# Kernel tuning notes

Hardware: AMD Instinct MI355X
Metric: run time of the kernel (lower is better)

## Reference

```python
import jax, jax.numpy as jnp
import numpy as np
from jax.ops import segment_sum

I_N, K_T, J_F, D, L, E, NT, H = 100000, 128, 64, 128, 2, 1000000, 500000, 2


def setup_inputs() -> dict:
    key = jax.random.key(0)
    ks = jax.random.split(key, 32)
    def rn(k, shp, s=0.02):
        return jax.random.normal(k, shp, jnp.float32) * s
    inp = {}
    inp["edge_x"] = jax.random.normal(ks[0], (E, J_F), jnp.float32)
    inp["edge_i"] = jax.random.randint(ks[1], (E,), 0, I_N, jnp.int32)
    inp["edge_k"] = jax.random.randint(ks[2], (E,), 0, K_T, jnp.int32)
    inp["idx_i"] = jax.random.randint(ks[3], (NT,), 0, I_N, jnp.int32)
    inp["idx_j"] = jax.random.randint(ks[4], (NT,), 0, J_F, jnp.int32)
    inp["idx_k"] = jax.random.randint(ks[5], (NT,), 0, K_T, jnp.int32)
    # parameters
    inp["u0"] = rn(ks[6], (I_N, D))          # Embedding(I,dim), xavier-ish
    inp["w0"] = rn(ks[7], (K_T, D), 0.01)
    inp["ep_W"] = rn(ks[8], (J_F, D))        # edge_proj (stored [in,out])
    inp["ep_b"] = jnp.zeros((D,), jnp.float32)
    inp["uW"] = rn(ks[9], (L, 2 * D, D))
    inp["ub"] = jnp.zeros((L, D), jnp.float32)
    inp["wW"] = rn(ks[10], (L, 2 * D, D))
    inp["wb"] = jnp.zeros((L, D), jnp.float32)
    inp["pos"] = rn(ks[11], (K_T, D), 0.01)
    inp["Wq"] = rn(ks[12], (D, D)); inp["Wk"] = rn(ks[13], (D, D)); inp["Wv"] = rn(ks[14], (D, D))
    inp["bq"] = jnp.zeros((D,), jnp.float32); inp["bk"] = jnp.zeros((D,), jnp.float32); inp["bv"] = jnp.zeros((D,), jnp.float32)
    inp["Wo"] = rn(ks[15], (D, D)); inp["bo"] = jnp.zeros((D,), jnp.float32)
    inp["ln1_g"] = jnp.ones((D,), jnp.float32); inp["ln1_b"] = jnp.zeros((D,), jnp.float32)
    inp["f_W1"] = rn(ks[16], (D, 4 * D)); inp["f_b1"] = jnp.zeros((4 * D,), jnp.float32)
    inp["f_W2"] = rn(ks[17], (4 * D, D)); inp["f_b2"] = jnp.zeros((D,), jnp.float32)
    inp["ln2_g"] = jnp.ones((D,), jnp.float32); inp["ln2_b"] = jnp.zeros((D,), jnp.float32)
    inp["V"] = rn(ks[18], (J_F, D))
    inp["bias"] = jnp.zeros((1,), jnp.float32)
    return inp


def _ln(x, g, b, eps=1e-5):
    m = jnp.mean(x, -1, keepdims=True)
    v = jnp.mean((x - m) ** 2, -1, keepdims=True)
    return (x - m) * jax.lax.rsqrt(v + eps) * g + b


def reference(edge_x, edge_i, edge_k, idx_i, idx_j, idx_k, u0, w0, ep_W, ep_b,
              uW, ub, wW, wb, pos, Wq, Wk, Wv, bq, bk, bv, Wo, bo,
              ln1_g, ln1_b, f_W1, f_b1, f_W2, f_b2, ln2_g, ln2_b, V, bias):
    I, K = u0.shape[0], w0.shape[0]
    e = edge_x @ ep_W + ep_b                                   # [E,D] edge_proj (same every layer)
    ones = jnp.ones((edge_i.shape[0],), jnp.float32)
    cnt_u = jnp.clip(segment_sum(ones, edge_i, num_segments=I), 1.0)[:, None]
    cnt_w = jnp.clip(segment_sum(ones, edge_k, num_segments=K), 1.0)[:, None]
    U, W = u0, w0
    for l in range(uW.shape[0]):
        U_msg = segment_sum(W[edge_k] + e, edge_i, num_segments=I)
        W_msg = segment_sum(U[edge_i] + e, edge_k, num_segments=K)
        U = jax.nn.relu(jnp.concatenate([U, U_msg / cnt_u], 1) @ uW[l] + ub[l])
        W = jax.nn.relu(jnp.concatenate([W, W_msg / cnt_w], 1) @ wW[l] + wb[l])
    # TimeRefine: MHA over K time tokens
    dh = D // H
    X = W + pos                                                # [K,D]
    q = (X @ Wq + bq).reshape(K, H, dh)
    k_ = (X @ Wk + bk).reshape(K, H, dh)
    v = (X @ Wv + bv).reshape(K, H, dh)
    scores = jnp.einsum('qhd,khd->hqk', q, k_) / jnp.sqrt(jnp.float32(dh))
    attn = jnp.einsum('hqk,khd->qhd', jax.nn.softmax(scores, -1), v).reshape(K, D)
    attn = attn @ Wo + bo
    H1 = _ln(X + attn, ln1_g, ln1_b)
    H2 = jax.nn.relu(H1 @ f_W1 + f_b1) @ f_W2 + f_b2
    Wf = _ln(H1 + H2, ln2_g, ln2_b)
    # decode triples
    s = U[idx_i] * Wf[idx_k]                                   # [N,D]
    out = jnp.sum(s * V[idx_j], -1) + bias[0]
    return jax.nn.sigmoid(out)
```

## Files before the change

kernel.cpp:

```cpp
#include <hip/hip_runtime.h>
#include <hip/hip_bf16.h>

#define D_DIM 128
#define KT 128
#define JF 64
#define WB_BLOCKS 256

typedef __attribute__((ext_vector_type(8))) short bf16x8;
typedef __attribute__((ext_vector_type(4))) float f32x4;

__device__ inline unsigned short f2b(float f) {
    __hip_bfloat16 h = __float2bfloat16(f);
    return *reinterpret_cast<unsigned short*>(&h);
}
__device__ inline float b2f(unsigned short u) {
    unsigned int x = ((unsigned int)u) << 16;
    return __uint_as_float(x);
}

__global__ void __launch_bounds__(256) edge_pass_kernel(
    const float* __restrict__ edge_x, const int* __restrict__ edge_i,
    const int* __restrict__ edge_k, float* __restrict__ Xi, float* __restrict__ Xk,
    unsigned* __restrict__ NmatP, unsigned* __restrict__ cntw, int E, int epb)
{
    __shared__ float xk_s[KT * JF];
    __shared__ unsigned cw_s[KT];
    for (int t = threadIdx.x; t < KT * JF; t += 256) xk_s[t] = 0.f;
    if (threadIdx.x < KT) cw_s[threadIdx.x] = 0u;
    __syncthreads();
    const int wid = threadIdx.x >> 6, lane = threadIdx.x & 63;
    const long base = (long)blockIdx.x * epb;
    for (int c = wid; c < epb; c += 4) {
        long e = base + c;
        if (e >= (long)E) break;
        int i = edge_i[e], k = edge_k[e];
        float x = edge_x[e * 64 + lane];
        unsafeAtomicAdd(&Xi[(long)i * 64 + lane], x);
        unsafeAtomicAdd(&xk_s[k * 64 + lane], x);
        if (lane == 0) atomicAdd(&NmatP[(long)i * 32 + (k >> 2)], 1u << ((k & 3) * 8));
        if (lane == 1) atomicAdd(&cw_s[k], 1u);
    }
    __syncthreads();
    for (int t = threadIdx.x; t < KT * JF; t += 256) {
        float v = xk_s[t];
        if (v != 0.f) unsafeAtomicAdd(&Xk[t], v);
    }
    if (threadIdx.x < KT && cw_s[threadIdx.x]) atomicAdd(&cntw[threadIdx.x], cw_s[threadIdx.x]);
}

__global__ void __launch_bounds__(256) mid_kernel(
    const unsigned* __restrict__ NmatP, float* __restrict__ cntraw,
    float* __restrict__ invcnt, int nNodes, int cntB,
    const float* __restrict__ u0, unsigned short* __restrict__ U0b, long n4,
    const float* __restrict__ uWt, const float* __restrict__ Wl,
    const float* __restrict__ uWb, const float* __restrict__ ep_W,
    const float* __restrict__ ep_b,
    unsigned short* __restrict__ Bt, float* __restrict__ ebx)
{
    const int bid = blockIdx.x;
    if (bid < cntB) {
        int row = bid * 4 + (threadIdx.x >> 6);
        int lane = threadIdx.x & 63;
        if (row < nNodes && lane < 32) {
            unsigned wv = NmatP[(long)row * 32 + lane];
            unsigned s = (wv & 0xFF) + ((wv >> 8) & 0xFF) + ((wv >> 16) & 0xFF) + (wv >> 24);
            #pragma unroll
            for (int o = 16; o; o >>= 1) s += __shfl_down(s, o, 32);
            if (lane == 0) {
                float c = (float)s;
                cntraw[row] = c;
                invcnt[row] = 1.f / fmaxf(c, 1.f);
            }
        }
    } else if (bid < cntB + 1024) {
        long i = (long)(bid - cntB) * 256 + threadIdx.x;
        long stride = (long)1024 * 256;
        for (; i < n4; i += stride) {
            float4 v = *(const float4*)&u0[i * 4];
            ushort4 o = make_ushort4(f2b(v.x), f2b(v.y), f2b(v.z), f2b(v.w));
            *(ushort4*)&U0b[i * 4] = o;
        }
    } else {
        int idx = (bid - cntB - 1024) * 256 + threadIdx.x;
        if (idx < 128 * 320) {
            int n = idx / 320, kk = idx - n * 320;
            float v;
            if (kk < 128) {
                v = uWt[kk * 128 + n];
            } else {
                const float* a = (kk < 256) ? (Wl + (kk - 128) * 128) : (ep_W + (kk - 256) * 128);
                float s = 0.f;
                #pragma unroll 8
                for (int j = 0; j < 128; ++j) s += a[j] * uWb[j * 128 + n];
                v = s;
            }
            Bt[idx] = f2b(v);
        } else if (idx < 128 * 320 + 128) {
            int n = idx - 128 * 320;
            float s = 0.f;
            #pragma unroll 8
            for (int j = 0; j < 128; ++j) s += ep_b[j] * uWb[j * 128 + n];
            ebx[n] = s;
        }
    }
}

__global__ void prep_kernel(const float* __restrict__ uWt, const float* __restrict__ Wl,
                            const float* __restrict__ uWb, const float* __restrict__ ep_W,
                            const float* __restrict__ ep_b,
                            unsigned short* __restrict__ Bt, float* __restrict__ ebx)
{
    int idx = blockIdx.x * 256 + threadIdx.x;
    if (idx < 128 * 320) {
        int n = idx / 320, kk = idx - n * 320;
        float v;
        if (kk < 128) {
            v = uWt[kk * 128 + n];
        } else {
            const float* a = (kk < 256) ? (Wl + (kk - 128) * 128) : (ep_W + (kk - 256) * 128);
            float s = 0.f;
            #pragma unroll 8
            for (int j = 0; j < 128; ++j) s += a[j] * uWb[j * 128 + n];
            v = s;
        }
        Bt[idx] = f2b(v);
    } else if (idx < 128 * 320 + 128) {
        int n = idx - 128 * 320;
        float s = 0.f;
        #pragma unroll 8
        for (int j = 0; j < 128; ++j) s += ep_b[j] * uWb[j * 128 + n];
        ebx[n] = s;
    }
}

__global__ void __launch_bounds__(256) layerA_mfma(
    const unsigned short* __restrict__ U_in, const unsigned char* __restrict__ Nmat8,
    const float* __restrict__ Xi, const float* __restrict__ cntraw,
    const float* __restrict__ invcnt, const unsigned short* __restrict__ Bt,
    const float* __restrict__ ub_l, const float* __restrict__ ebx,
    unsigned short* __restrict__ U_out, int nNodes)
{
    __shared__ __align__(16) unsigned short A_s[128][40];
    __shared__ __align__(16) unsigned short B_s[128][40];
    const int tid = threadIdx.x;
    const int w = tid >> 6, lane = tid & 63;
    const int quad = lane >> 4, l16 = lane & 15;
    const int nodeBase = blockIdx.x * 128;
    f32x4 acc[2][8];
    #pragma unroll
    for (int a = 0; a < 2; ++a)
        #pragma unroll
        for (int b = 0; b < 8; ++b) acc[a][b] = (f32x4){0.f, 0.f, 0.f, 0.f};

    const int rr = tid >> 3;
    const int kc = (tid & 7) * 4;

    for (int ks = 0; ks < 10; ++ks) {
        const int k0 = ks * 32;
        __syncthreads();
        {
            int n = tid & 127, seg = tid >> 7;
            const unsigned short* src = Bt + n * 320 + k0 + seg * 16;
            uint4 p0 = *(const uint4*)(src);
            uint4 p1 = *(const uint4*)(src + 8);
            *(uint4*)&B_s[n][seg * 16]     = p0;
            *(uint4*)&B_s[n][seg * 16 + 8] = p1;
        }
        #pragma unroll
        for (int p = 0; p < 4; ++p) {
            int r = p * 32 + rr;
            int node = nodeBase + r;
            ushort4 w4 = make_ushort4(0, 0, 0, 0);
            if (node < nNodes) {
                if (ks < 4) {
                    w4 = *(const ushort4*)&U_in[(long)node * 128 + k0 + kc];
                } else if (ks < 8) {
                    float inv = invcnt[node];
                    const unsigned char* np_ = &Nmat8[(long)node * 128 + (k0 - 128) + kc];
                    w4 = make_ushort4(f2b((float)np_[0] * inv), f2b((float)np_[1] * inv),
                                      f2b((float)np_[2] * inv), f2b((float)np_[3] * inv));
                } else {
                    float inv = invcnt[node];
                    float4 x = *(const float4*)&Xi[(long)node * 64 + (k0 - 256) + kc];
                    w4 = make_ushort4(f2b(x.x * inv), f2b(x.y * inv),
                                      f2b(x.z * inv), f2b(x.w * inv));
                }
            }
            *(ushort4*)&A_s[r][kc] = w4;
        }
        __syncthreads();
        bf16x8 a0 = *(const bf16x8*)&A_s[w * 32 + l16][quad * 8];
        bf16x8 a1 = *(const bf16x8*)&A_s[w * 32 + 16 + l16][quad * 8];
        #pragma unroll
        for (int nt = 0; nt < 8; ++nt) {
            bf16x8 b = *(const bf16x8*)&B_s[nt * 16 + l16][quad * 8];
            acc[0][nt] = __builtin_amdgcn_mfma_f32_16x16x32_bf16(a0, b, acc[0][nt], 0, 0, 0);
            acc[1][nt] = __builtin_amdgcn_mfma_f32_16x16x32_bf16(a1, b, acc[1][nt], 0, 0, 0);
        }
    }
    #pragma unroll
    for (int mt = 0; mt < 2; ++mt) {
        #pragma unroll
        for (int r = 0; r < 4; ++r) {
            int row = w * 32 + mt * 16 + quad * 4 + r;
            int node = nodeBase + row;
            if (node < nNodes) {
                float flag = (cntraw[node] > 0.f) ? 1.f : 0.f;
                #pragma unroll
                for (int nt = 0; nt < 8; ++nt) {
                    int col = nt * 16 + l16;
                    float vv = acc[mt][nt][r] + ub_l[col] + flag * ebx[col];
                    U_out[(long)node * 128 + col] = f2b(fmaxf(vv, 0.f));
                }
            }
        }
    }
}

__global__ void __launch_bounds__(256) wmsgB_mfma(
    const unsigned short* __restrict__ U, const unsigned char* __restrict__ Nmat8,
    float* __restrict__ partial, int nodes_per_block, int nNodes)
{
    __shared__ __align__(16) unsigned short A_s[128][40];
    __shared__ __align__(16) unsigned short B_s[128][40];
    const int tid = threadIdx.x;
    const int w = tid >> 6, lane = tid & 63;
    const int quad = lane >> 4, l16 = lane & 15;
    f32x4 acc[2][8];
    #pragma unroll
    for (int a = 0; a < 2; ++a)
        #pragma unroll
        for (int b = 0; b < 8; ++b) acc[a][b] = (f32x4){0.f, 0.f, 0.f, 0.f};

    int base = blockIdx.x * nodes_per_block;
    int end = min(base + nodes_per_block, nNodes);
    const int nn = tid >> 3;
    const int cc = (tid & 7) * 16;
    for (int g = base; g < end; g += 32) {
        int cnt = min(32, end - g);
        __syncthreads();
        if (nn < cnt) {
            int node = g + nn;
            uint4 nb = *(const uint4*)&Nmat8[(long)node * 128 + cc];
            const unsigned char* nbp = (const unsigned char*)&nb;
            uint4 ua = *(const uint4*)&U[(long)node * 128 + cc];
            uint4 ubb = *(const uint4*)&U[(long)node * 128 + cc + 8];
            unsigned short uv[16];
            *(uint4*)&uv[0] = ua;
            *(uint4*)&uv[8] = ubb;
            #pragma unroll
            for (int j = 0; j < 16; ++j) {
                A_s[cc + j][nn] = f2b((float)nbp[j]);
                B_s[cc + j][nn] = uv[j];
            }
        } else {
            #pragma unroll
            for (int j = 0; j < 16; ++j) { A_s[cc + j][nn] = 0; B_s[cc + j][nn] = 0; }
        }
        __syncthreads();
        bf16x8 a0 = *(const bf16x8*)&A_s[w * 32 + l16][quad * 8];
        bf16x8 a1 = *(const bf16x8*)&A_s[w * 32 + 16 + l16][quad * 8];
        #pragma unroll
        for (int nt = 0; nt < 8; ++nt) {
            bf16x8 b = *(const bf16x8*)&B_s[nt * 16 + l16][quad * 8];
            acc[0][nt] = __builtin_amdgcn_mfma_f32_16x16x32_bf16(a0, b, acc[0][nt], 0, 0, 0);
            acc[1][nt] = __builtin_amdgcn_mfma_f32_16x16x32_bf16(a1, b, acc[1][nt], 0, 0, 0);
        }
    }
    float* my = partial + (size_t)blockIdx.x * 16384;
    #pragma unroll
    for (int mt = 0; mt < 2; ++mt)
        #pragma unroll
        for (int r = 0; r < 4; ++r) {
            int row = w * 32 + mt * 16 + quad * 4 + r;
            #pragma unroll
            for (int nt = 0; nt < 8; ++nt)
                my[row * 128 + nt * 16 + l16] = acc[mt][nt][r];
        }
}

__global__ void __launch_bounds__(128) wfin_gemm_kernel(
    const float* __restrict__ partial, const float* __restrict__ Xk,
    const unsigned* __restrict__ cntw, const float* __restrict__ ep_W,
    const float* __restrict__ ep_b, const float* __restrict__ Wrow,
    const float* __restrict__ wWt, const float* __restrict__ wWb,
    const float* __restrict__ wb_l, float* __restrict__ Wout)
{
    __shared__ float msg_s[128];
    __shared__ float a_s[128];
    const int kk = blockIdx.x, t = threadIdx.x;
    float c = (float)cntw[kk];
    {
        float s = 0.f;
        const float* pp = partial + kk * 128 + t;
        #pragma unroll 8
        for (int b = 0; b < WB_BLOCKS; ++b) s += pp[(size_t)b * 16384];
        const float* xk = Xk + kk * 64;
        #pragma unroll 8
        for (int j = 0; j < 64; ++j) s += xk[j] * ep_W[j * 128 + t];
        s += c * ep_b[t];
        msg_s[t] = s / fmaxf(c, 1.f);
        a_s[t] = Wrow[kk * 128 + t];
    }
    __syncthreads();
    float s = wb_l[t];
    #pragma unroll 4
    for (int k = 0; k < 128; ++k) s += a_s[k] * wWt[k * 128 + t];
    #pragma unroll 4
    for (int k = 0; k < 128; ++k) s += msg_s[k] * wWb[k * 128 + t];
    Wout[kk * 128 + t] = fmaxf(s, 0.f);
}

__global__ void qkvf_kernel(const float* __restrict__ W2, const float* __restrict__ pos,
                            const float* __restrict__ Wq, const float* __restrict__ Wk,
                            const float* __restrict__ Wv, const float* __restrict__ bq,
                            const float* __restrict__ bk, const float* __restrict__ bv,
                            float* __restrict__ Xmat,
                            float* __restrict__ qm, float* __restrict__ km, float* __restrict__ vm)
{
    int idx = blockIdx.x * 256 + threadIdx.x;
    if (idx >= 128 * 384) return;
    int m = idx / 384, c = idx - m * 384;
    int sel = c >> 7, n = c & 127;
    const float* W = (sel == 0) ? Wq : (sel == 1) ? Wk : Wv;
    const float* b = (sel == 0) ? bq : (sel == 1) ? bk : bv;
    float s = b[n];
    const float* x2 = W2 + m * 128;
    const float* xp = pos + m * 128;
    #pragma unroll 8
    for (int k = 0; k < 128; ++k) s += (x2[k] + xp[k]) * W[k * 128 + n];
    float* o = (sel == 0) ? qm : (sel == 1) ? km : vm;
    o[m * 128 + n] = s;
    if (sel == 0) Xmat[m * 128 + n] = x2[n] + xp[n];
}

__global__ void __launch_bounds__(128) attn_tail_kernel(
    const float* __restrict__ q, const float* __restrict__ kmat,
    const float* __restrict__ vmat, const float* __restrict__ Wo,
    const float* __restrict__ bo, const float* __restrict__ Xmat,
    const float* __restrict__ ln1_g, const float* __restrict__ ln1_b,
    const float* __restrict__ f_W1, const float* __restrict__ f_b1,
    const float* __restrict__ f_W2, const float* __restrict__ f_b2,
    const float* __restrict__ ln2_g, const float* __restrict__ ln2_b,
    float* __restrict__ Wf)
{
    __shared__ float p_s[128];
    __shared__ float a_s[128];
    __shared__ float h1_s[128];
    __shared__ float f_s[512];
    __shared__ float red_s[4];
    const int tok = blockIdx.x;
    const int t = threadIdx.x;
    const int lane = t & 63, wid = t >> 6;
    for (int h = 0; h < 2; ++h) {
        const float* qr = q + tok * 128 + h * 64;
        const float* kr = kmat + t * 128 + h * 64;
        float s = 0.f;
        #pragma unroll
        for (int d = 0; d < 64; ++d) s += qr[d] * kr[d];
        s *= 0.125f;
        float m = s;
        #pragma unroll
        for (int o = 32; o; o >>= 1) m = fmaxf(m, __shfl_down(m, o, 64));
        if (lane == 0) red_s[wid] = m;
        __syncthreads();
        m = fmaxf(red_s[0], red_s[1]);
        float ev = expf(s - m);
        float ss = ev;
        #pragma unroll
        for (int o = 32; o; o >>= 1) ss += __shfl_down(ss, o, 64);
        if (lane == 0) red_s[2 + wid] = ss;
        __syncthreads();
        float tot = red_s[2] + red_s[3];
        p_s[t] = ev / tot;
        __syncthreads();
        if (t < 64) {
            float o = 0.f;
            #pragma unroll 8
            for (int j = 0; j < 128; ++j) o += p_s[j] * vmat[j * 128 + h * 64 + t];
            a_s[h * 64 + t] = o;
        }
        __syncthreads();
    }
    {
        float v = bo[t];
        #pragma unroll 4
        for (int k = 0; k < 128; ++k) v += a_s[k] * Wo[k * 128 + t];
        v += Xmat[tok * 128 + t];
        float s = v;
        #pragma unroll
        for (int o = 32; o; o >>= 1) s += __shfl_down(s, o, 64);
        if (lane == 0) red_s[wid] = s;
        __syncthreads();
        float mean = (red_s[0] + red_s[1]) * (1.f / 128.f);
        float d = v - mean;
        float q2 = d * d;
        #pragma unroll
        for (int o = 32; o; o >>= 1) q2 += __shfl_down(q2, o, 64);
        if (lane == 0) red_s[2 + wid] = q2;
        __syncthreads();
        float var = (red_s[2] + red_s[3]) * (1.f / 128.f);
        h1_s[t] = d * rsqrtf(var + 1e-5f) * ln1_g[t] + ln1_b[t];
        __syncthreads();
    }
    #pragma unroll
    for (int nn = 0; nn < 4; ++nn) {
        int n = t + nn * 128;
        float s = f_b1[n];
        #pragma unroll 4
        for (int k = 0; k < 128; ++k) s += h1_s[k] * f_W1[k * 512 + n];
        f_s[n] = fmaxf(s, 0.f);
    }
    __syncthreads();
    float v = f_b2[t];
    #pragma unroll 4
    for (int k = 0; k < 512; ++k) v += f_s[k] * f_W2[k * 128 + t];
    v += h1_s[t];
    float s = v;
    #pragma unroll
    for (int o = 32; o; o >>= 1) s += __shfl_down(s, o, 64);
    if (lane == 0) red_s[wid] = s;
    __syncthreads();
    float mean = (red_s[0] + red_s[1]) * (1.f / 128.f);
    float d = v - mean;
    float q2 = d * d;
    #pragma unroll
    for (int o = 32; o; o >>= 1) q2 += __shfl_down(q2, o, 64);
    if (lane == 0) red_s[2 + wid] = q2;
    __syncthreads();
    float var = (red_s[2] + red_s[3]) * (1.f / 128.f);
    Wf[tok * 128 + t] = d * rsqrtf(var + 1e-5f) * ln2_g[t] + ln2_b[t];
}

__global__ void __launch_bounds__(256) decode_kernel(
    const int* __restrict__ idx_i, const int* __restrict__ idx_j, const int* __restrict__ idx_k,
    const unsigned short* __restrict__ U2, const float* __restrict__ Wf, const float* __restrict__ V,
    const float* __restrict__ bias, float* __restrict__ out, int n)
{
    const int g = threadIdx.x >> 4;
    const int hl = threadIdx.x & 15;
    int t = blockIdx.x * 16 + g;
    if (t >= n) return;
    int i = idx_i[t], j = idx_j[t], kk = idx_k[t];
    const unsigned short* up = U2 + (long)i * 128 + hl * 8;
    const float* wp = Wf + kk * 128 + hl * 8;
    const float* vp = V + j * 128 + hl * 8;
    uint4 ur = *(const uint4*)up;
    const unsigned short* uu = (const unsigned short*)&ur;
    float4 w0 = *(const float4*)wp,  w1 = *(const float4*)(wp + 4);
    float4 v0 = *(const float4*)vp,  v1 = *(const float4*)(vp + 4);
    float s = b2f(uu[0]) * w0.x * v0.x + b2f(uu[1]) * w0.y * v0.y
            + b2f(uu[2]) * w0.z * v0.z + b2f(uu[3]) * w0.w * v0.w
            + b2f(uu[4]) * w1.x * v1.x + b2f(uu[5]) * w1.y * v1.y
            + b2f(uu[6]) * w1.z * v1.z + b2f(uu[7]) * w1.w * v1.w;
    #pragma unroll
    for (int o = 8; o; o >>= 1) s += __shfl_down(s, o, 16);
    if (hl == 0) out[t] = 1.f / (1.f + expf(-(s + bias[0])));
}

extern "C" void kernel_launch(void* const* d_in, const int* in_sizes, int n_in,
                              void* d_out, int out_size, void* d_ws, size_t ws_size,
                              hipStream_t stream)
{
    const float* edge_x = (const float*)d_in[0];
    const int*   edge_i = (const int*)d_in[1];
    const int*   edge_k = (const int*)d_in[2];
    const int*   idx_i  = (const int*)d_in[3];
    const int*   idx_j  = (const int*)d_in[4];
    const int*   idx_k  = (const int*)d_in[5];
    const float* u0   = (const float*)d_in[6];
    const float* w0   = (const float*)d_in[7];
    const float* ep_W = (const float*)d_in[8];
    const float* ep_b = (const float*)d_in[9];
    const float* uW   = (const float*)d_in[10];
    const float* ub   = (const float*)d_in[11];
    const float* wW   = (const float*)d_in[12];
    const float* wb   = (const float*)d_in[13];
    const float* pos  = (const float*)d_in[14];
    const float* Wq = (const float*)d_in[15];
    const float* Wk = (const float*)d_in[16];
    const float* Wv = (const float*)d_in[17];
    const float* bq = (const float*)d_in[18];
    const float* bk = (const float*)d_in[19];
    const float* bv = (const float*)d_in[20];
    const float* Wo = (const float*)d_in[21];
    const float* bo = (const float*)d_in[22];
    const float* ln1_g = (const float*)d_in[23];
    const float* ln1_b = (const float*)d_in[24];
    const float* f_W1 = (const float*)d_in[25];
    const float* f_b1 = (const float*)d_in[26];
    const float* f_W2 = (const float*)d_in[27];
    const float* f_b2 = (const float*)d_in[28];
    const float* ln2_g = (const float*)d_in[29];
    const float* ln2_b = (const float*)d_in[30];
    const float* Vmat = (const float*)d_in[31];
    const float* bias = (const float*)d_in[32];

    const int E   = in_sizes[1];
    const int NTt = in_sizes[3];
    const int nNodes = in_sizes[6] / D_DIM;

    char* ws = (char*)d_ws;
    size_t off = 0;
    auto alloc = [&](size_t bytes) -> char* {
        char* p = ws + off;
        off = (off + bytes + 255) & ~(size_t)255;
        return p;
    };
    unsigned* NmatP  = (unsigned*)alloc((size_t)nNodes * 32 * 4);
    float*    Xi     = (float*)alloc((size_t)nNodes * 64 * 4);
    float*    Xkseg  = (float*)alloc(128 * 64 * 4);
    unsigned* cntw   = (unsigned*)alloc(512);
    size_t zeroBytes = off;
    float* cntraw = (float*)alloc((size_t)nNodes * 4);
    float* invcnt = (float*)alloc((size_t)nNodes * 4);
    unsigned short* U0b = (unsigned short*)alloc((size_t)nNodes * 128 * 2);
    unsigned short* U1b = (unsigned short*)alloc((size_t)nNodes * 128 * 2);
    unsigned short* U2b = (unsigned short*)alloc((size_t)nNodes * 128 * 2);
    float* partials = (float*)alloc((size_t)WB_BLOCKS * 16384 * 4);
    unsigned short* Bt0 = (unsigned short*)alloc(128 * 320 * 2);
    unsigned short* Bt1 = (unsigned short*)alloc(128 * 320 * 2);
    float* W1 = (float*)alloc(65536);
    float* W2 = (float*)alloc(65536);
    float* ebx0 = (float*)alloc(512);
    float* ebx1 = (float*)alloc(512);
    float* Xmat  = (float*)alloc(65536);
    float* qm    = (float*)alloc(65536);
    float* km    = (float*)alloc(65536);
    float* vm    = (float*)alloc(65536);
    float* Wfm   = (float*)alloc(65536);

    const unsigned char* Nmat8 = (const unsigned char*)NmatP;

    const float* uWt0 = uW;
    const float* uWb0 = uW + 128 * 128;
    const float* uWt1 = uW + 256 * 128;
    const float* uWb1 = uW + 256 * 128 + 128 * 128;
    const float* wWt0 = wW;
    const float* wWb0 = wW + 128 * 128;
    const float* wWt1 = wW + 256 * 128;
    const float* wWb1 = wW + 256 * 128 + 128 * 128;

    hipMemsetAsync(d_ws, 0, zeroBytes, stream);

    int epb = (E + 1023) / 1024;
    edge_pass_kernel<<<1024, 256, 0, stream>>>(edge_x, edge_i, edge_k, Xi, Xkseg,
                                               NmatP, cntw, E, epb);

    int cntB = (nNodes + 3) / 4;
    mid_kernel<<<cntB + 1024 + 161, 256, 0, stream>>>(
        NmatP, cntraw, invcnt, nNodes, cntB,
        u0, U0b, (long)nNodes * 32,
        uWt0, w0, uWb0, ep_W, ep_b, Bt0, ebx0);

    int npb = (nNodes + WB_BLOCKS - 1) / WB_BLOCKS;
    int la_grid = (nNodes + 127) / 128;

    wmsgB_mfma<<<WB_BLOCKS, 256, 0, stream>>>(U0b, Nmat8, partials, npb, nNodes);
    layerA_mfma<<<la_grid, 256, 0, stream>>>(U0b, Nmat8, Xi, cntraw, invcnt, Bt0, ub, ebx0, U1b, nNodes);
    wfin_gemm_kernel<<<128, 128, 0, stream>>>(partials, Xkseg, cntw, ep_W, ep_b,
                                              w0, wWt0, wWb0, wb, W1);

    prep_kernel<<<161, 256, 0, stream>>>(uWt1, W1, uWb1, ep_W, ep_b, Bt1, ebx1);
    wmsgB_mfma<<<WB_BLOCKS, 256, 0, stream>>>(U1b, Nmat8, partials, npb, nNodes);
    layerA_mfma<<<la_grid, 256, 0, stream>>>(U1b, Nmat8, Xi, cntraw, invcnt, Bt1, ub + 128, ebx1, U2b, nNodes);
    wfin_gemm_kernel<<<128, 128, 0, stream>>>(partials, Xkseg, cntw, ep_W, ep_b,
                                              W1, wWt1, wWb1, wb + 128, W2);

    qkvf_kernel<<<192, 256, 0, stream>>>(W2, pos, Wq, Wk, Wv, bq, bk, bv, Xmat, qm, km, vm);
    attn_tail_kernel<<<128, 128, 0, stream>>>(qm, km, vm, Wo, bo, Xmat, ln1_g, ln1_b,
                                              f_W1, f_b1, f_W2, f_b2, ln2_g, ln2_b, Wfm);

    decode_kernel<<<(NTt + 15) / 16, 256, 0, stream>>>(idx_i, idx_j, idx_k, U2b, Wfm, Vmat,
                                                       bias, (float*)d_out, NTt);
}
```

Measured before the change: 1.139 ms.

## Fuse edge pass with prep, merge wmsg/layerA kernels, bf16 packed atomics for Xi

The edge scatter is merged with the u0 bf16 conversion and the weight-prep work for both layers into one launch. The counting step is split into its own small kernel. The W-message and U-layer MFMA kernels are combined into a single dual-role grid. Xi is now accumulated with packed bf16 atomics, which halves atomic traffic and footprint but lowers accumulation precision. Layer-1 Bt prep now happens inside wfin_gemm, which removes the separate prep launch and lets independent work overlap instead of running serially.

```diff
diff --git a/kernel.cpp b/kernel.cpp
--- a/kernel.cpp
+++ b/kernel.cpp
@@ -18,112 +18,35 @@
     return __uint_as_float(x);
 }
 
-__global__ void __launch_bounds__(256) edge_pass_kernel(
-    const float* __restrict__ edge_x, const int* __restrict__ edge_i,
-    const int* __restrict__ edge_k, float* __restrict__ Xi, float* __restrict__ Xk,
-    unsigned* __restrict__ NmatP, unsigned* __restrict__ cntw, int E, int epb)
-{
-    __shared__ float xk_s[KT * JF];
-    __shared__ unsigned cw_s[KT];
-    for (int t = threadIdx.x; t < KT * JF; t += 256) xk_s[t] = 0.f;
-    if (threadIdx.x < KT) cw_s[threadIdx.x] = 0u;
-    __syncthreads();
-    const int wid = threadIdx.x >> 6, lane = threadIdx.x & 63;
-    const long base = (long)blockIdx.x * epb;
-    for (int c = wid; c < epb; c += 4) {
-        long e = base + c;
-        if (e >= (long)E) break;
-        int i = edge_i[e], k = edge_k[e];
-        float x = edge_x[e * 64 + lane];
-        unsafeAtomicAdd(&Xi[(long)i * 64 + lane], x);
-        unsafeAtomicAdd(&xk_s[k * 64 + lane], x);
-        if (lane == 0) atomicAdd(&NmatP[(long)i * 32 + (k >> 2)], 1u << ((k & 3) * 8));
-        if (lane == 1) atomicAdd(&cw_s[k], 1u);
-    }
-    __syncthreads();
-    for (int t = threadIdx.x; t < KT * JF; t += 256) {
-        float v = xk_s[t];
-        if (v != 0.f) unsafeAtomicAdd(&Xk[t], v);
-    }
-    if (threadIdx.x < KT && cw_s[threadIdx.x]) atomicAdd(&cntw[threadIdx.x], cw_s[threadIdx.x]);
-}
-
-__global__ void __launch_bounds__(256) mid_kernel(
-    const unsigned* __restrict__ NmatP, float* __restrict__ cntraw,
-    float* __restrict__ invcnt, int nNodes, int cntB,
-    const float* __restrict__ u0, unsigned short* __restrict__ U0b, long n4,
-    const float* __restrict__ uWt, const float* __restrict__ Wl,
-    const float* __restrict__ uWb, const float* __restrict__ ep_W,
-    const float* __restrict__ ep_b,
-    unsigned short* __restrict__ Bt, float* __restrict__ ebx)
-{
-    const int bid = blockIdx.x;
-    if (bid < cntB) {
-        int row = bid * 4 + (threadIdx.x >> 6);
-        int lane = threadIdx.x & 63;
-        if (row < nNodes && lane < 32) {
-            unsigned wv = NmatP[(long)row * 32 + lane];
-            unsigned s = (wv & 0xFF) + ((wv >> 8) & 0xFF) + ((wv >> 16) & 0xFF) + (wv >> 24);
-            #pragma unroll
-            for (int o = 16; o; o >>= 1) s += __shfl_down(s, o, 32);
-            if (lane == 0) {
-                float c = (float)s;
-                cntraw[row] = c;
-                invcnt[row] = 1.f / fmaxf(c, 1.f);
-            }
-        }
-    } else if (bid < cntB + 1024) {
-        long i = (long)(bid - cntB) * 256 + threadIdx.x;
-        long stride = (long)1024 * 256;
-        for (; i < n4; i += stride) {
-            float4 v = *(const float4*)&u0[i * 4];
-            ushort4 o = make_ushort4(f2b(v.x), f2b(v.y), f2b(v.z), f2b(v.w));
-            *(ushort4*)&U0b[i * 4] = o;
-        }
-    } else {
-        int idx = (bid - cntB - 1024) * 256 + threadIdx.x;
-        if (idx < 128 * 320) {
-            int n = idx / 320, kk = idx - n * 320;
-            float v;
-            if (kk < 128) {
-                v = uWt[kk * 128 + n];
-            } else {
-                const float* a = (kk < 256) ? (Wl + (kk - 128) * 128) : (ep_W + (kk - 256) * 128);
+__device__ inline void atomPkAddBf16(unsigned short* addr, unsigned packed) {
+    asm volatile("global_atomic_pk_add_bf16 %0, %1, off"
+                 :: "v"(addr), "v"(packed) : "memory");
+}
+
+__device__ inline void prep_body(int idx, const float* uWt, const float* Wl,
+                                 const float* uWb, const float* ep_W,
+                                 const float* ep_b, unsigned short* Bt,
+                                 float* ebx)
+{
+    if (idx < 128 * 320) {
+        int n = idx / 320, kk = idx - n * 320;
+        if (kk < 128) {
+            Bt[idx] = f2b(uWt[kk * 128 + n]);
+        } else if (kk < 256) {
+            if (Wl) {
+                const float* a = Wl + (kk - 128) * 128;
                 float s = 0.f;
                 #pragma unroll 8
                 for (int j = 0; j < 128; ++j) s += a[j] * uWb[j * 128 + n];
-                v = s;
-            }
-            Bt[idx] = f2b(v);
-        } else if (idx < 128 * 320 + 128) {
-            int n = idx - 128 * 320;
-            float s = 0.f;
-            #pragma unroll 8
-            for (int j = 0; j < 128; ++j) s += ep_b[j] * uWb[j * 128 + n];
-            ebx[n] = s;
-        }
-    }
-}
-
-__global__ void prep_kernel(const float* __restrict__ uWt, const float* __restrict__ Wl,
-                            const float* __restrict__ uWb, const float* __restrict__ ep_W,
-                            const float* __restrict__ ep_b,
-                            unsigned short* __restrict__ Bt, float* __restrict__ ebx)
-{
-    int idx = blockIdx.x * 256 + threadIdx.x;
-    if (idx < 128 * 320) {
-        int n = idx / 320, kk = idx - n * 320;
-        float v;
-        if (kk < 128) {
-            v = uWt[kk * 128 + n];
+                Bt[idx] = f2b(s);
+            }
         } else {
-            const float* a = (kk < 256) ? (Wl + (kk - 128) * 128) : (ep_W + (kk - 256) * 128);
+            const float* a = ep_W + (kk - 256) * 128;
             float s = 0.f;
             #pragma unroll 8
             for (int j = 0; j < 128; ++j) s += a[j] * uWb[j * 128 + n];
-            v = s;
-        }
-        Bt[idx] = f2b(v);
+            Bt[idx] = f2b(s);
+        }
     } else if (idx < 128 * 320 + 128) {
         int n = idx - 128 * 320;
         float s = 0.f;
@@ -133,93 +56,88 @@
     }
 }
 
-__global__ void __launch_bounds__(256) layerA_mfma(
+__global__ void __launch_bounds__(256) edge_fused_kernel(
+    const float* __restrict__ edge_x, const int* __restrict__ edge_i,
+    const int* __restrict__ edge_k, unsigned short* __restrict__ XiB,
+    float* __restrict__ Xk, unsigned* __restrict__ NmatP,
+    unsigned* __restrict__ cntw, int E, int epb,
+    const float* __restrict__ u0, unsigned short* __restrict__ U0b, long n4,
+    const float* __restrict__ uWt0, const float* __restrict__ w0,
+    const float* __restrict__ uWb0, const float* __restrict__ uWt1,
+    const float* __restrict__ uWb1, const float* __restrict__ ep_W,
+    const float* __restrict__ ep_b,
+    unsigned short* __restrict__ Bt0, float* __restrict__ ebx0,
+    unsigned short* __restrict__ Bt1, float* __restrict__ ebx1)
+{
+    __shared__ float xk_s[KT * JF];
+    __shared__ unsigned cw_s[KT];
+    const unsigned bid = blockIdx.x;
+    if (bid < 1024) {
+        for (int t = threadIdx.x; t < KT * JF; t += 256) xk_s[t] = 0.f;
+        if (threadIdx.x < KT) cw_s[threadIdx.x] = 0u;
+        __syncthreads();
+        const int wid = threadIdx.x >> 6, lane = threadIdx.x & 63;
+        const int half = lane >> 5, l2 = lane & 31;
+        const long base = (long)bid * epb;
+        for (int c = wid * 2 + half; c < epb; c += 8) {
+            long e = base + c;
+            if (e >= (long)E) break;
+            int i = edge_i[e], k = edge_k[e];
+            float2 x2 = *(const float2*)&edge_x[e * 64 + l2 * 2];
+            unsigned pk = ((unsigned)f2b(x2.y) << 16) | (unsigned)f2b(x2.x);
+            atomPkAddBf16(&XiB[(long)i * 64 + l2 * 2], pk);
+            unsafeAtomicAdd(&xk_s[k * 64 + l2 * 2], x2.x);
+            unsafeAtomicAdd(&xk_s[k * 64 + l2 * 2 + 1], x2.y);
+            if (l2 == 0) atomicAdd(&NmatP[(long)i * 32 + (k >> 2)], 1u << ((k & 3) * 8));
+            if (l2 == 1) atomicAdd(&cw_s[k], 1u);
+        }
+        asm volatile("s_waitcnt vmcnt(0)" ::: "memory");
+        __syncthreads();
+        for (int t = threadIdx.x; t < KT * JF; t += 256) {
+            float v = xk_s[t];
+            if (v != 0.f) unsafeAtomicAdd(&Xk[t], v);
+        }
+        if (threadIdx.x < KT && cw_s[threadIdx.x]) atomicAdd(&cntw[threadIdx.x], cw_s[threadIdx.x]);
+    } else if (bid < 2048) {
+        long i = (long)(bid - 1024) * 256 + threadIdx.x;
+        long stride = (long)1024 * 256;
+        for (; i < n4; i += stride) {
+            float4 v = *(const float4*)&u0[i * 4];
+            ushort4 o = make_ushort4(f2b(v.x), f2b(v.y), f2b(v.z), f2b(v.w));
+            *(ushort4*)&U0b[i * 4] = o;
+        }
+    } else if (bid < 2209) {
+        prep_body((int)(bid - 2048) * 256 + threadIdx.x, uWt0, w0, uWb0, ep_W, ep_b, Bt0, ebx0);
+    } else {
+        prep_body((int)(bid - 2209) * 256 + threadIdx.x, uWt1, nullptr, uWb1, ep_W, ep_b, Bt1, ebx1);
+    }
+}
+
+__global__ void __launch_bounds__(256) cnt_kernel(
+    const unsigned* __restrict__ NmatP, float* __restrict__ cntraw,
+    float* __restrict__ invcnt, int nNodes)
+{
+    int row = blockIdx.x * 4 + (threadIdx.x >> 6);
+    int lane = threadIdx.x & 63;
+    if (row >= nNodes || lane >= 32) return;
+    unsigned wv = NmatP[(long)row * 32 + lane];
+    unsigned s = (wv & 0xFF) + ((wv >> 8) & 0xFF) + ((wv >> 16) & 0xFF) + (wv >> 24);
+    #pragma unroll
+    for (int o = 16; o; o >>= 1) s += __shfl_down(s, o, 32);
+    if (lane == 0) {
+        float c = (float)s;
+        cntraw[row] = c;
+        invcnt[row] = 1.f / fmaxf(c, 1.f);
+    }
+}
+
+__global__ void __launch_bounds__(256) dual_mfma(
     const unsigned short* __restrict__ U_in, const unsigned char* __restrict__ Nmat8,
-    const float* __restrict__ Xi, const float* __restrict__ cntraw,
+    float* __restrict__ partial, int nodes_per_block,
+    const unsigned short* __restrict__ XiB, const float* __restrict__ cntraw,
     const float* __restrict__ invcnt, const unsigned short* __restrict__ Bt,
     const float* __restrict__ ub_l, const float* __restrict__ ebx,
-    unsigned short* __restrict__ U_out, int nNodes)
-{
-    __shared__ __align__(16) unsigned short A_s[128][40];
-    __shared__ __align__(16) unsigned short B_s[128][40];
-    const int tid = threadIdx.x;
-    const int w = tid >> 6, lane = tid & 63;
-    const int quad = lane >> 4, l16 = lane & 15;
-    const int nodeBase = blockIdx.x * 128;
-    f32x4 acc[2][8];
-    #pragma unroll
-    for (int a = 0; a < 2; ++a)
-        #pragma unroll
-        for (int b = 0; b < 8; ++b) acc[a][b] = (f32x4){0.f, 0.f, 0.f, 0.f};
-
-    const int rr = tid >> 3;
-    const int kc = (tid & 7) * 4;
-
-    for (int ks = 0; ks < 10; ++ks) {
-        const int k0 = ks * 32;
-        __syncthreads();
-        {
-            int n = tid & 127, seg = tid >> 7;
-            const unsigned short* src = Bt + n * 320 + k0 + seg * 16;
-            uint4 p0 = *(const uint4*)(src);
-            uint4 p1 = *(const uint4*)(src + 8);
-            *(uint4*)&B_s[n][seg * 16]     = p0;
-            *(uint4*)&B_s[n][seg * 16 + 8] = p1;
-        }
-        #pragma unroll
-        for (int p = 0; p < 4; ++p) {
-            int r = p * 32 + rr;
-            int node = nodeBase + r;
-            ushort4 w4 = make_ushort4(0, 0, 0, 0);
-            if (node < nNodes) {
-                if (ks < 4) {
-                    w4 = *(const ushort4*)&U_in[(long)node * 128 + k0 + kc];
-                } else if (ks < 8) {
-                    float inv = invcnt[node];
-                    const unsigned char* np_ = &Nmat8[(long)node * 128 + (k0 - 128) + kc];
-                    w4 = make_ushort4(f2b((float)np_[0] * inv), f2b((float)np_[1] * inv),
-                                      f2b((float)np_[2] * inv), f2b((float)np_[3] * inv));
-                } else {
-                    float inv = invcnt[node];
-                    float4 x = *(const float4*)&Xi[(long)node * 64 + (k0 - 256) + kc];
-                    w4 = make_ushort4(f2b(x.x * inv), f2b(x.y * inv),
-                                      f2b(x.z * inv), f2b(x.w * inv));
-                }
-            }
-            *(ushort4*)&A_s[r][kc] = w4;
-        }
-        __syncthreads();
-        bf16x8 a0 = *(const bf16x8*)&A_s[w * 32 + l16][quad * 8];
-        bf16x8 a1 = *(const bf16x8*)&A_s[w * 32 + 16 + l16][quad * 8];
-        #pragma unroll
-        for (int nt = 0; nt < 8; ++nt) {
-            bf16x8 b = *(const bf16x8*)&B_s[nt * 16 + l16][quad * 8];
-            acc[0][nt] = __builtin_amdgcn_mfma_f32_16x16x32_bf16(a0, b, acc[0][nt], 0, 0, 0);
-            acc[1][nt] = __builtin_amdgcn_mfma_f32_16x16x32_bf16(a1, b, acc[1][nt], 0, 0, 0);
-        }
-    }
-    #pragma unroll
-    for (int mt = 0; mt < 2; ++mt) {
-        #pragma unroll
-        for (int r = 0; r < 4; ++r) {
-            int row = w * 32 + mt * 16 + quad * 4 + r;
-            int node = nodeBase + row;
-            if (node < nNodes) {
-                float flag = (cntraw[node] > 0.f) ? 1.f : 0.f;
-                #pragma unroll
-                for (int nt = 0; nt < 8; ++nt) {
-                    int col = nt * 16 + l16;
-                    float vv = acc[mt][nt][r] + ub_l[col] + flag * ebx[col];
-                    U_out[(long)node * 128 + col] = f2b(fmaxf(vv, 0.f));
-                }
-            }
-        }
-    }
-}
-
-__global__ void __launch_bounds__(256) wmsgB_mfma(
-    const unsigned short* __restrict__ U, const unsigned char* __restrict__ Nmat8,
-    float* __restrict__ partial, int nodes_per_block, int nNodes)
+    unsigned short* __restrict__ U_out, int nNodes, int wbB)
 {
     __shared__ __align__(16) unsigned short A_s[128][40];
     __shared__ __align__(16) unsigned short B_s[128][40];
@@ -232,51 +150,117 @@
         #pragma unroll
         for (int b = 0; b < 8; ++b) acc[a][b] = (f32x4){0.f, 0.f, 0.f, 0.f};
 
-    int base = blockIdx.x * nodes_per_block;
-    int end = min(base + nodes_per_block, nNodes);
-    const int nn = tid >> 3;
-    const int cc = (tid & 7) * 16;
-    for (int g = base; g < end; g += 32) {
-        int cnt = min(32, end - g);
-        __syncthreads();
-        if (nn < cnt) {
-            int node = g + nn;
-            uint4 nb = *(const uint4*)&Nmat8[(long)node * 128 + cc];
-            const unsigned char* nbp = (const unsigned char*)&nb;
-            uint4 ua = *(const uint4*)&U[(long)node * 128 + cc];
-            uint4 ubb = *(const uint4*)&U[(long)node * 128 + cc + 8];
-            unsigned short uv[16];
-            *(uint4*)&uv[0] = ua;
-            *(uint4*)&uv[8] = ubb;
+    if ((int)blockIdx.x < wbB) {
+        int base = blockIdx.x * nodes_per_block;
+        int end = min(base + nodes_per_block, nNodes);
+        const int nn = tid >> 3;
+        const int cc = (tid & 7) * 16;
+        for (int g = base; g < end; g += 32) {
+            int cnt = min(32, end - g);
+            __syncthreads();
+            if (nn < cnt) {
+                int node = g + nn;
+                uint4 nb = *(const uint4*)&Nmat8[(long)node * 128 + cc];
+                const unsigned char* nbp = (const unsigned char*)&nb;
+                uint4 ua = *(const uint4*)&U_in[(long)node * 128 + cc];
+                uint4 ubb = *(const uint4*)&U_in[(long)node * 128 + cc + 8];
+                unsigned short uv[16];
+                *(uint4*)&uv[0] = ua;
+                *(uint4*)&uv[8] = ubb;
+                #pragma unroll
+                for (int j = 0; j < 16; ++j) {
+                    A_s[cc + j][nn] = f2b((float)nbp[j]);
+                    B_s[cc + j][nn] = uv[j];
+                }
+            } else {
+                #pragma unroll
+                for (int j = 0; j < 16; ++j) { A_s[cc + j][nn] = 0; B_s[cc + j][nn] = 0; }
+            }
+            __syncthreads();
+            bf16x8 a0 = *(const bf16x8*)&A_s[w * 32 + l16][quad * 8];
+            bf16x8 a1 = *(const bf16x8*)&A_s[w * 32 + 16 + l16][quad * 8];
             #pragma unroll
-            for (int j = 0; j < 16; ++j) {
-                A_s[cc + j][nn] = f2b((float)nbp[j]);
-                B_s[cc + j][nn] = uv[j];
-            }
-        } else {
+            for (int nt = 0; nt < 8; ++nt) {
+                bf16x8 b = *(const bf16x8*)&B_s[nt * 16 + l16][quad * 8];
+                acc[0][nt] = __builtin_amdgcn_mfma_f32_16x16x32_bf16(a0, b, acc[0][nt], 0, 0, 0);
+                acc[1][nt] = __builtin_amdgcn_mfma_f32_16x16x32_bf16(a1, b, acc[1][nt], 0, 0, 0);
+            }
+        }
+        float* my = partial + (size_t)blockIdx.x * 16384;
+        #pragma unroll
+        for (int mt = 0; mt < 2; ++mt)
             #pragma unroll
-            for (int j = 0; j < 16; ++j) { A_s[cc + j][nn] = 0; B_s[cc + j][nn] = 0; }
-        }
-        __syncthreads();
-        bf16x8 a0 = *(const bf16x8*)&A_s[w * 32 + l16][quad * 8];
-        bf16x8 a1 = *(const bf16x8*)&A_s[w * 32 + 16 + l16][quad * 8];
-        #pragma unroll
-        for (int nt = 0; nt < 8; ++nt) {
-            bf16x8 b = *(const bf16x8*)&B_s[nt * 16 + l16][quad * 8];
-            acc[0][nt] = __builtin_amdgcn_mfma_f32_16x16x32_bf16(a0, b, acc[0][nt], 0, 0, 0);
-            acc[1][nt] = __builtin_amdgcn_mfma_f32_16x16x32_bf16(a1, b, acc[1][nt], 0, 0, 0);
-        }
-    }
-    float* my = partial + (size_t)blockIdx.x * 16384;
-    #pragma unroll
-    for (int mt = 0; mt < 2; ++mt)
-        #pragma unroll
-        for (int r = 0; r < 4; ++r) {
-            int row = w * 32 + mt * 16 + quad * 4 + r;
+            for (int r = 0; r < 4; ++r) {
+                int row = w * 32 + mt * 16 + quad * 4 + r;
+                #pragma unroll
+                for (int nt = 0; nt < 8; ++nt)
+                    my[row * 128 + nt * 16 + l16] = acc[mt][nt][r];
+            }
+    } else {
+        const int nodeBase = ((int)blockIdx.x - wbB) * 128;
+        const int rr = tid >> 3;
+        const int kc = (tid & 7) * 4;
+        for (int ks = 0; ks < 10; ++ks) {
+            const int k0 = ks * 32;
+            __syncthreads();
+            {
+                int n = tid & 127, seg = tid >> 7;
+                const unsigned short* src = Bt + n * 320 + k0 + seg * 16;
+                uint4 p0 = *(const uint4*)(src);
+                uint4 p1 = *(const uint4*)(src + 8);
+                *(uint4*)&B_s[n][seg * 16]     = p0;
+                *(uint4*)&B_s[n][seg * 16 + 8] = p1;
+            }
             #pragma unroll
-            for (int nt = 0; nt < 8; ++nt)
-                my[row * 128 + nt * 16 + l16] = acc[mt][nt][r];
-        }
+            for (int p = 0; p < 4; ++p) {
+                int r = p * 32 + rr;
+                int node = nodeBase + r;
+                ushort4 w4 = make_ushort4(0, 0, 0, 0);
+                if (node < nNodes) {
+                    if (ks < 4) {
+                        w4 = *(const ushort4*)&U_in[(long)node * 128 + k0 + kc];
+                    } else if (ks < 8) {
+                        float inv = invcnt[node];
+                        const unsigned char* np_ = &Nmat8[(long)node * 128 + (k0 - 128) + kc];
+                        w4 = make_ushort4(f2b((float)np_[0] * inv), f2b((float)np_[1] * inv),
+                                          f2b((float)np_[2] * inv), f2b((float)np_[3] * inv));
+                    } else {
+                        float inv = invcnt[node];
+                        ushort4 x = *(const ushort4*)&XiB[(long)node * 64 + (k0 - 256) + kc];
+                        w4 = make_ushort4(f2b(b2f(x.x) * inv), f2b(b2f(x.y) * inv),
+                                          f2b(b2f(x.z) * inv), f2b(b2f(x.w) * inv));
+                    }
+                }
+                *(ushort4*)&A_s[r][kc] = w4;
+            }
+            __syncthreads();
+            bf16x8 a0 = *(const bf16x8*)&A_s[w * 32 + l16][quad * 8];
+            bf16x8 a1 = *(const bf16x8*)&A_s[w * 32 + 16 + l16][quad * 8];
+            #pragma unroll
+            for (int nt = 0; nt < 8; ++nt) {
+                bf16x8 b = *(const bf16x8*)&B_s[nt * 16 + l16][quad * 8];
+                acc[0][nt] = __builtin_amdgcn_mfma_f32_16x16x32_bf16(a0, b, acc[0][nt], 0, 0, 0);
+                acc[1][nt] = __builtin_amdgcn_mfma_f32_16x16x32_bf16(a1, b, acc[1][nt], 0, 0, 0);
+            }
+        }
+        #pragma unroll
+        for (int mt = 0; mt < 2; ++mt) {
+            #pragma unroll
+            for (int r = 0; r < 4; ++r) {
+                int row = w * 32 + mt * 16 + quad * 4 + r;
+                int node = nodeBase + row;
+                if (node < nNodes) {
+                    float flag = (cntraw[node] > 0.f) ? 1.f : 0.f;
+                    #pragma unroll
+                    for (int nt = 0; nt < 8; ++nt) {
+                        int col = nt * 16 + l16;
+                        float vv = acc[mt][nt][r] + ub_l[col] + flag * ebx[col];
+                        U_out[(long)node * 128 + col] = f2b(fmaxf(vv, 0.f));
+                    }
+                }
+            }
+        }
+    }
 }
 
 __global__ void __launch_bounds__(128) wfin_gemm_kernel(
@@ -284,10 +268,12 @@
     const unsigned* __restrict__ cntw, const float* __restrict__ ep_W,
     const float* __restrict__ ep_b, const float* __restrict__ Wrow,
     const float* __restrict__ wWt, const float* __restrict__ wWb,
-    const float* __restrict__ wb_l, float* __restrict__ Wout)
+    const float* __restrict__ wb_l, float* __restrict__ Wout,
+    const float* __restrict__ uWb_next, unsigned short* __restrict__ Bt_next)
 {
     __shared__ float msg_s[128];
     __shared__ float a_s[128];
+    __shared__ float w_s[128];
     const int kk = blockIdx.x, t = threadIdx.x;
     float c = (float)cntw[kk];
     {
@@ -308,7 +294,16 @@
     for (int k = 0; k < 128; ++k) s += a_s[k] * wWt[k * 128 + t];
     #pragma unroll 4
     for (int k = 0; k < 128; ++k) s += msg_s[k] * wWb[k * 128 + t];
-    Wout[kk * 128 + t] = fmaxf(s, 0.f);
+    float wv = fmaxf(s, 0.f);
+    Wout[kk * 128 + t] = wv;
+    if (Bt_next) {
+        w_s[t] = wv;
+        __syncthreads();
+        float bt = 0.f;
+        #pragma unroll 4
+        for (int j = 0; j < 128; ++j) bt += w_s[j] * uWb_next[j * 128 + t];
+        Bt_next[t * 320 + 128 + kk] = f2b(bt);
+    }
 }
 
 __global__ void qkvf_kernel(const float* __restrict__ W2, const float* __restrict__ pos,
@@ -508,7 +503,7 @@
         return p;
     };
     unsigned* NmatP  = (unsigned*)alloc((size_t)nNodes * 32 * 4);
-    float*    Xi     = (float*)alloc((size_t)nNodes * 64 * 4);
+    unsigned short* XiB = (unsigned short*)alloc((size_t)nNodes * 64 * 2);
     float*    Xkseg  = (float*)alloc(128 * 64 * 4);
     unsigned* cntw   = (unsigned*)alloc(512);
     size_t zeroBytes = off;
@@ -544,28 +539,25 @@
     hipMemsetAsync(d_ws, 0, zeroBytes, stream);
 
     int epb = (E + 1023) / 1024;
-    edge_pass_kernel<<<1024, 256, 0, stream>>>(edge_x, edge_i, edge_k, Xi, Xkseg,
-                                               NmatP, cntw, E, epb);
-
-    int cntB = (nNodes + 3) / 4;
-    mid_kernel<<<cntB + 1024 + 161, 256, 0, stream>>>(
-        NmatP, cntraw, invcnt, nNodes, cntB,
+    edge_fused_kernel<<<2370, 256, 0, stream>>>(
+        edge_x, edge_i, edge_k, XiB, Xkseg, NmatP, cntw, E, epb,
         u0, U0b, (long)nNodes * 32,
-        uWt0, w0, uWb0, ep_W, ep_b, Bt0, ebx0);
+        uWt0, w0, uWb0, uWt1, uWb1, ep_W, ep_b, Bt0, ebx0, Bt1, ebx1);
+
+    cnt_kernel<<<(nNodes + 3) / 4, 256, 0, stream>>>(NmatP, cntraw, invcnt, nNodes);
 
     int npb = (nNodes + WB_BLOCKS - 1) / WB_BLOCKS;
     int la_grid = (nNodes + 127) / 128;
 
-    wmsgB_mfma<<<WB_BLOCKS, 256, 0, stream>>>(U0b, Nmat8, partials, npb, nNodes);
-    layerA_mfma<<<la_grid, 256, 0, stream>>>(U0b, Nmat8, Xi, cntraw, invcnt, Bt0, ub, ebx0, U1b, nNodes);
+    dual_mfma<<<WB_BLOCKS + la_grid, 256, 0, stream>>>(
+        U0b, Nmat8, partials, npb, XiB, cntraw, invcnt, Bt0, ub, ebx0, U1b, nNodes, WB_BLOCKS);
     wfin_gemm_kernel<<<128, 128, 0, stream>>>(partials, Xkseg, cntw, ep_W, ep_b,
-                                              w0, wWt0, wWb0, wb, W1);
-
-    prep_kernel<<<161, 256, 0, stream>>>(uWt1, W1, uWb1, ep_W, ep_b, Bt1, ebx1);
-    wmsgB_mfma<<<WB_BLOCKS, 256, 0, stream>>>(U1b, Nmat8, partials, npb, nNodes);
-    layerA_mfma<<<la_grid, 256, 0, stream>>>(U1b, Nmat8, Xi, cntraw, invcnt, Bt1, ub + 128, ebx1, U2b, nNodes);
+                                              w0, wWt0, wWb0, wb, W1, uWb1, Bt1);
+
+    dual_mfma<<<WB_BLOCKS + la_grid, 256, 0, stream>>>(
+        U1b, Nmat8, partials, npb, XiB, cntraw, invcnt, Bt1, ub + 128, ebx1, U2b, nNodes, WB_BLOCKS);
     wfin_gemm_kernel<<<128, 128, 0, stream>>>(partials, Xkseg, cntw, ep_W, ep_b,
-                                              W1, wWt1, wWb1, wb + 128, W2);
+                                              W1, wWt1, wWb1, wb + 128, W2, nullptr, nullptr);
 
     qkvf_kernel<<<192, 256, 0, stream>>>(W2, pos, Wq, Wk, Wv, bq, bk, bv, Xmat, qm, km, vm);
     attn_tail_kernel<<<128, 128, 0, stream>>>(qm, km, vm, Wo, bo, Xmat, ln1_g, ln1_b,
```

Result: faster. 1.077 ms (-5.5%).
